# Kernel tuning notes

Hardware: AMD Instinct MI355X
Metric: run time of the kernel (lower is better)

The kernel has to match this reference:

```python
import jax, jax.numpy as jnp
import numpy as np

LN_EPS = 1e-12


def setup_inputs() -> dict:
    key = jax.random.key(0)
    ks = jax.random.split(key, 6)
    B, S, H = 32, 512, 768
    P, K = 76, 64
    V, E = 50257, 768
    return {
        "sequence_data": jax.random.normal(ks[0], (B, S, H), dtype=jnp.float32),
        "masked_positions": jax.random.randint(ks[1], (B, P), 0, S, dtype=jnp.int64),
        "candidate_sets": jax.random.randint(ks[2], (B, P, K), 0, V, dtype=jnp.int64),
        "embedding_table": jax.random.normal(ks[3], (V, E), dtype=jnp.float32) * 0.02,
        "dense_w": jax.random.normal(ks[4], (H, E), dtype=jnp.float32) * (1.0 / np.sqrt(H)),
        "dense_b": jnp.zeros((E,), dtype=jnp.float32),
        "ln_gamma": jnp.ones((E,), dtype=jnp.float32),
        "ln_beta": jnp.zeros((E,), dtype=jnp.float32),
    }


def reference(sequence_data, masked_positions, candidate_sets, embedding_table,
              dense_w, dense_b, ln_gamma, ln_beta):
    # Gather masked positions: [B, P, H]
    gathered = jnp.take_along_axis(
        sequence_data, masked_positions[:, :, None], axis=1)
    # Dense (no activation), then LayerNorm (eps=1e-12)
    lm = jnp.einsum('bph,he->bpe', gathered, dense_w) + dense_b
    mu = jnp.mean(lm, axis=-1, keepdims=True)
    var = jnp.mean(jnp.square(lm - mu), axis=-1, keepdims=True)
    lm = (lm - mu) * jax.lax.rsqrt(var + LN_EPS) * ln_gamma + ln_beta
    # Candidate embedding gather: [B, P, K, E]
    cand = embedding_table[candidate_sets]
    # Inner products -> logits [B, P, K]
    logits = jnp.einsum('bpe,bpke->bpk', lm, cand)
    return logits
```

## Files before the change

kernel.cpp:

```cpp
#include <hip/hip_runtime.h>

typedef __attribute__((ext_vector_type(8))) short bf16x8;
typedef __attribute__((ext_vector_type(4))) float f32x4;

#define HH 768
#define EE 768
#define BB 32
#define SS 512
#define PP 76
#define KCAND 64
#define MM (BB * PP)
#define VV 50257

#define OFF_WT    0u
#define OFF_AG    1179648u
#define OFF_LM    4915200u

#define WT_BLOCKS 576
#define AG_BLOCKS 304
#define GEMM_BLOCKS 456

__device__ inline unsigned short f2bf(float f) {
    unsigned int u = __float_as_uint(f);
    u += 0x7fffu + ((u >> 16) & 1u);
    return (unsigned short)(u >> 16);
}
__device__ inline float bf2f(unsigned short h) {
    return __uint_as_float(((unsigned int)h) << 16);
}

__global__ __launch_bounds__(256) void prep_kernel(
    const float* __restrict__ W, unsigned short* __restrict__ Wt,
    const float* __restrict__ seq, const int* __restrict__ mpos,
    unsigned short* __restrict__ Ag) {
    const int bid = blockIdx.x;
    if (bid < WT_BLOCKS) {
        __shared__ float tile[32][33];
        const int h0 = (bid % 24) * 32, e0 = (bid / 24) * 32;
        const int c = threadIdx.x & 31, r = threadIdx.x >> 5;
#pragma unroll
        for (int rr = r; rr < 32; rr += 8)
            tile[rr][c] = W[(size_t)(h0 + rr) * EE + e0 + c];
        __syncthreads();
#pragma unroll
        for (int rr = r; rr < 32; rr += 8)
            Wt[(size_t)(e0 + rr) * HH + h0 + c] = f2bf(tile[c][rr]);
    } else {
        const int m0 = (bid - WT_BLOCKS) * 8;
        const int t = threadIdx.x;
#pragma unroll
        for (int rr = 0; rr < 8; ++rr) {
            const int m = m0 + rr;
            const int b = m / PP, p = m - b * PP;
            const int ps = mpos[b * PP + p];
            const float* srow = seq + (size_t)(b * SS + ps) * HH;
            unsigned short* drow = Ag + (size_t)m * HH;
#pragma unroll
            for (int j = 0; j < 3; ++j)
                drow[t + j * 256] = f2bf(srow[t + j * 256]);
        }
    }
}

__global__ __launch_bounds__(256) void gemm_kernel(
    const unsigned short* __restrict__ Ag, const unsigned short* __restrict__ Wt,
    float* __restrict__ lm) {
    __shared__ unsigned short Alds[64][72];
    __shared__ unsigned short Blds[64][72];
    const int bid = blockIdx.x;
    const int bn = bid % 12, bm = bid / 12;
    const int tid = threadIdx.x;
    const int sr = tid >> 2, sc = (tid & 3) * 16;
    const unsigned short* abase = Ag + (size_t)(bm * 64) * HH;
    const unsigned short* bbase = Wt + (size_t)(bn * 64) * HH;
    const int lane = tid & 63, wv = tid >> 6;
    const int wm = wv >> 1, wn = wv & 1;
    const int fr = lane & 15, fq = (lane >> 4) * 8;
    f32x4 acc[2][2] = {};
    for (int kk = 0; kk < HH; kk += 64) {
        __syncthreads();
        *(int4*)&Alds[sr][sc]     = *(const int4*)(abase + (size_t)sr * HH + kk + sc);
        *(int4*)&Alds[sr][sc + 8] = *(const int4*)(abase + (size_t)sr * HH + kk + sc + 8);
        *(int4*)&Blds[sr][sc]     = *(const int4*)(bbase + (size_t)sr * HH + kk + sc);
        *(int4*)&Blds[sr][sc + 8] = *(const int4*)(bbase + (size_t)sr * HH + kk + sc + 8);
        __syncthreads();
#pragma unroll
        for (int ks = 0; ks < 64; ks += 32) {
            bf16x8 af[2], bfr[2];
#pragma unroll
            for (int t = 0; t < 2; ++t)
                af[t] = *(const bf16x8*)&Alds[wm * 32 + t * 16 + fr][ks + fq];
#pragma unroll
            for (int t = 0; t < 2; ++t)
                bfr[t] = *(const bf16x8*)&Blds[wn * 32 + t * 16 + fr][ks + fq];
#pragma unroll
            for (int tm = 0; tm < 2; ++tm)
#pragma unroll
                for (int tn = 0; tn < 2; ++tn)
                    acc[tm][tn] = __builtin_amdgcn_mfma_f32_16x16x32_bf16(
                        af[tm], bfr[tn], acc[tm][tn], 0, 0, 0);
        }
    }
#pragma unroll
    for (int tm = 0; tm < 2; ++tm)
#pragma unroll
        for (int tn = 0; tn < 2; ++tn) {
            const int col = bn * 64 + wn * 32 + tn * 16 + (lane & 15);
            const int rbase = bm * 64 + wm * 32 + tm * 16 + (lane >> 4) * 4;
#pragma unroll
            for (int g = 0; g < 4; ++g)
                lm[(size_t)(rbase + g) * EE + col] = acc[tm][tn][g];
        }
}

__global__ __launch_bounds__(256, 2) void mrow_logits_kernel(
    const float* __restrict__ lm, const float* __restrict__ bias,
    const float* __restrict__ gamma, const float* __restrict__ beta,
    const int* __restrict__ cand, const float* __restrict__ emb,
    float* __restrict__ out) {
    const int m = blockIdx.x;
    const int t = threadIdx.x;
    __shared__ unsigned short lmn_s[EE];
    __shared__ float redS[4], redQ[4];
    __shared__ int cand_s[KCAND];

    if (t < KCAND) cand_s[t] = cand[m * KCAND + t];

    const float x0 = lm[(size_t)m * EE + t]       + bias[t];
    const float x1 = lm[(size_t)m * EE + t + 256] + bias[t + 256];
    const float x2 = lm[(size_t)m * EE + t + 512] + bias[t + 512];
    float s = x0 + x1 + x2;
    float q = x0 * x0 + x1 * x1 + x2 * x2;
#pragma unroll
    for (int w = 32; w; w >>= 1) { s += __shfl_xor(s, w); q += __shfl_xor(q, w); }
    const int lane = t & 63, wv = t >> 6;
    if (lane == 0) { redS[wv] = s; redQ[wv] = q; }
    __syncthreads();
    s = redS[0] + redS[1] + redS[2] + redS[3];
    q = redQ[0] + redQ[1] + redQ[2] + redQ[3];
    const float mu = s * (1.0f / 768.0f);
    const float rstd = rsqrtf(q * (1.0f / 768.0f) - mu * mu + 1e-12f);
    lmn_s[t]       = f2bf((x0 - mu) * rstd * gamma[t]       + beta[t]);
    lmn_s[t + 256] = f2bf((x1 - mu) * rstd * gamma[t + 256] + beta[t + 256]);
    lmn_s[t + 512] = f2bf((x2 - mu) * rstd * gamma[t + 512] + beta[t + 512]);
    __syncthreads();

    const int g = t >> 4, l16 = t & 15;
    ushort4 ln4[12];
#pragma unroll
    for (int j = 0; j < 12; ++j)
        ln4[j] = *(const ushort4*)&lmn_s[4 * l16 + 64 * j];

    const f32x4* e4 = (const f32x4*)emb;
    const int cb = m * KCAND + g;
    const f32x4* p0 = e4 + (size_t)cand_s[g]      * 192 + l16;
    const f32x4* p1 = e4 + (size_t)cand_s[g + 16] * 192 + l16;
    const f32x4* p2 = e4 + (size_t)cand_s[g + 32] * 192 + l16;
    const f32x4* p3 = e4 + (size_t)cand_s[g + 48] * 192 + l16;
    f32x4 A0[12], A1[12], A2[12], A3[12];
#pragma unroll
    for (int j = 0; j < 12; ++j) A0[j] = p0[16 * j];
#pragma unroll
    for (int j = 0; j < 12; ++j) A1[j] = p1[16 * j];
#pragma unroll
    for (int j = 0; j < 12; ++j) A2[j] = p2[16 * j];
#pragma unroll
    for (int j = 0; j < 12; ++j) A3[j] = p3[16 * j];
    __builtin_amdgcn_sched_barrier(0);

    float d0 = 0.f, d1 = 0.f, d2 = 0.f, d3 = 0.f;
    float f0 = 0.f, f1 = 0.f, f2 = 0.f, f3 = 0.f;
#pragma unroll
    for (int j = 0; j < 12; j += 2) {
        float la[4], lb[4];
        la[0] = bf2f(ln4[j].x);     la[1] = bf2f(ln4[j].y);
        la[2] = bf2f(ln4[j].z);     la[3] = bf2f(ln4[j].w);
        lb[0] = bf2f(ln4[j + 1].x); lb[1] = bf2f(ln4[j + 1].y);
        lb[2] = bf2f(ln4[j + 1].z); lb[3] = bf2f(ln4[j + 1].w);
        d0 += la[0]*A0[j][0] + la[1]*A0[j][1] + la[2]*A0[j][2] + la[3]*A0[j][3];
        d1 += la[0]*A1[j][0] + la[1]*A1[j][1] + la[2]*A1[j][2] + la[3]*A1[j][3];
        d2 += la[0]*A2[j][0] + la[1]*A2[j][1] + la[2]*A2[j][2] + la[3]*A2[j][3];
        d3 += la[0]*A3[j][0] + la[1]*A3[j][1] + la[2]*A3[j][2] + la[3]*A3[j][3];
        f0 += lb[0]*A0[j+1][0] + lb[1]*A0[j+1][1] + lb[2]*A0[j+1][2] + lb[3]*A0[j+1][3];
        f1 += lb[0]*A1[j+1][0] + lb[1]*A1[j+1][1] + lb[2]*A1[j+1][2] + lb[3]*A1[j+1][3];
        f2 += lb[0]*A2[j+1][0] + lb[1]*A2[j+1][1] + lb[2]*A2[j+1][2] + lb[3]*A2[j+1][3];
        f3 += lb[0]*A3[j+1][0] + lb[1]*A3[j+1][1] + lb[2]*A3[j+1][2] + lb[3]*A3[j+1][3];
    }
    d0 += f0; d1 += f1; d2 += f2; d3 += f3;
#pragma unroll
    for (int w = 1; w < 16; w <<= 1) {
        d0 += __shfl_xor(d0, w); d1 += __shfl_xor(d1, w);
        d2 += __shfl_xor(d2, w); d3 += __shfl_xor(d3, w);
    }
    if (l16 == 0) {
        out[cb]      = d0;
        out[cb + 16] = d1;
        out[cb + 32] = d2;
        out[cb + 48] = d3;
    }
}

extern "C" void kernel_launch(void* const* d_in, const int* in_sizes, int n_in,
                              void* d_out, int out_size, void* d_ws, size_t ws_size,
                              hipStream_t stream) {
    const float* seq   = (const float*)d_in[0];
    const int*   mpos  = (const int*)d_in[1];
    const int*   cand  = (const int*)d_in[2];
    const float* emb   = (const float*)d_in[3];
    const float* W     = (const float*)d_in[4];
    const float* bias  = (const float*)d_in[5];
    const float* gamma = (const float*)d_in[6];
    const float* beta  = (const float*)d_in[7];
    float* out = (float*)d_out;

    char* ws = (char*)d_ws;
    unsigned short* Wt = (unsigned short*)(ws + OFF_WT);
    unsigned short* Ag = (unsigned short*)(ws + OFF_AG);
    float*          lm = (float*)(ws + OFF_LM);

    prep_kernel<<<WT_BLOCKS + AG_BLOCKS, 256, 0, stream>>>(W, Wt, seq, mpos, Ag);
    gemm_kernel<<<GEMM_BLOCKS, 256, 0, stream>>>(Ag, Wt, lm);
    mrow_logits_kernel<<<MM, 256, 0, stream>>>(lm, bias, gamma, beta, cand, emb, out);
}
```

Before: 292.0 us.

## Convert embedding table to bf16 alongside GEMM and gather bf16 rows

Adds conversion blocks to the GEMM launch that cast the full fp32 embedding table to bf16 in workspace. The logits kernel then gathers candidate rows as bf16 vectors, halving bytes per gathered row. This trades a full-table streaming read and write each call for cheaper random gathers, and it adds bf16 rounding on the embeddings. The logits kernel also drops its occupancy hint.

```diff
diff --git a/kernel.cpp b/kernel.cpp
--- a/kernel.cpp
+++ b/kernel.cpp
@@ -15,10 +15,12 @@
 #define OFF_WT    0u
 #define OFF_AG    1179648u
 #define OFF_LM    4915200u
+#define OFF_EMB   12386304u
 
 #define WT_BLOCKS 576
 #define AG_BLOCKS 304
 #define GEMM_BLOCKS 456
+#define CONV_BLOCKS 18847
 
 __device__ inline unsigned short f2bf(float f) {
     unsigned int u = __float_as_uint(f);
@@ -62,12 +64,25 @@
     }
 }
 
-__global__ __launch_bounds__(256) void gemm_kernel(
+__global__ __launch_bounds__(256) void gemm_conv_kernel(
     const unsigned short* __restrict__ Ag, const unsigned short* __restrict__ Wt,
-    float* __restrict__ lm) {
-    __shared__ unsigned short Alds[64][72];
-    __shared__ unsigned short Blds[64][72];
+    float* __restrict__ lm, const float* __restrict__ embf,
+    unsigned short* __restrict__ embB) {
     const int bid = blockIdx.x;
+    if (bid >= GEMM_BLOCKS) {
+        const size_t i = ((size_t)(bid - GEMM_BLOCKS) * 2048) + (size_t)threadIdx.x * 8;
+        if (i < (size_t)VV * EE) {
+            const float4 a = *(const float4*)(embf + i);
+            const float4 b = *(const float4*)(embf + i + 4);
+            unsigned short o[8];
+            o[0] = f2bf(a.x); o[1] = f2bf(a.y); o[2] = f2bf(a.z); o[3] = f2bf(a.w);
+            o[4] = f2bf(b.x); o[5] = f2bf(b.y); o[6] = f2bf(b.z); o[7] = f2bf(b.w);
+            *(int4*)(embB + i) = *(const int4*)o;
+        }
+        return;
+    }
+    __shared__ __align__(16) unsigned short Alds[64][72];
+    __shared__ __align__(16) unsigned short Blds[64][72];
     const int bn = bid % 12, bm = bid / 12;
     const int tid = threadIdx.x;
     const int sr = tid >> 2, sc = (tid & 3) * 16;
@@ -113,14 +128,14 @@
         }
 }
 
-__global__ __launch_bounds__(256, 2) void mrow_logits_kernel(
+__global__ __launch_bounds__(256) void mrow_logits_kernel(
     const float* __restrict__ lm, const float* __restrict__ bias,
     const float* __restrict__ gamma, const float* __restrict__ beta,
-    const int* __restrict__ cand, const float* __restrict__ emb,
+    const int* __restrict__ cand, const unsigned short* __restrict__ embB,
     float* __restrict__ out) {
     const int m = blockIdx.x;
     const int t = threadIdx.x;
-    __shared__ unsigned short lmn_s[EE];
+    __shared__ __align__(16) unsigned short lmn_s[EE];
     __shared__ float redS[4], redQ[4];
     __shared__ int cand_s[KCAND];
 
@@ -146,45 +161,49 @@
     __syncthreads();
 
     const int g = t >> 4, l16 = t & 15;
-    ushort4 ln4[12];
-#pragma unroll
-    for (int j = 0; j < 12; ++j)
-        ln4[j] = *(const ushort4*)&lmn_s[4 * l16 + 64 * j];
-
-    const f32x4* e4 = (const f32x4*)emb;
+    bf16x8 ln8[6];
+#pragma unroll
+    for (int j = 0; j < 6; ++j)
+        ln8[j] = *(const bf16x8*)&lmn_s[8 * l16 + 128 * j];
+
+    const bf16x8* e8 = (const bf16x8*)embB;
     const int cb = m * KCAND + g;
-    const f32x4* p0 = e4 + (size_t)cand_s[g]      * 192 + l16;
-    const f32x4* p1 = e4 + (size_t)cand_s[g + 16] * 192 + l16;
-    const f32x4* p2 = e4 + (size_t)cand_s[g + 32] * 192 + l16;
-    const f32x4* p3 = e4 + (size_t)cand_s[g + 48] * 192 + l16;
-    f32x4 A0[12], A1[12], A2[12], A3[12];
-#pragma unroll
-    for (int j = 0; j < 12; ++j) A0[j] = p0[16 * j];
-#pragma unroll
-    for (int j = 0; j < 12; ++j) A1[j] = p1[16 * j];
-#pragma unroll
-    for (int j = 0; j < 12; ++j) A2[j] = p2[16 * j];
-#pragma unroll
-    for (int j = 0; j < 12; ++j) A3[j] = p3[16 * j];
+    const bf16x8* p0 = e8 + (size_t)cand_s[g]      * 96 + l16;
+    const bf16x8* p1 = e8 + (size_t)cand_s[g + 16] * 96 + l16;
+    const bf16x8* p2 = e8 + (size_t)cand_s[g + 32] * 96 + l16;
+    const bf16x8* p3 = e8 + (size_t)cand_s[g + 48] * 96 + l16;
+    bf16x8 A0[6], A1[6], A2[6], A3[6];
+#pragma unroll
+    for (int j = 0; j < 6; ++j) A0[j] = p0[16 * j];
+#pragma unroll
+    for (int j = 0; j < 6; ++j) A1[j] = p1[16 * j];
+#pragma unroll
+    for (int j = 0; j < 6; ++j) A2[j] = p2[16 * j];
+#pragma unroll
+    for (int j = 0; j < 6; ++j) A3[j] = p3[16 * j];
     __builtin_amdgcn_sched_barrier(0);
 
     float d0 = 0.f, d1 = 0.f, d2 = 0.f, d3 = 0.f;
     float f0 = 0.f, f1 = 0.f, f2 = 0.f, f3 = 0.f;
 #pragma unroll
-    for (int j = 0; j < 12; j += 2) {
-        float la[4], lb[4];
-        la[0] = bf2f(ln4[j].x);     la[1] = bf2f(ln4[j].y);
-        la[2] = bf2f(ln4[j].z);     la[3] = bf2f(ln4[j].w);
-        lb[0] = bf2f(ln4[j + 1].x); lb[1] = bf2f(ln4[j + 1].y);
-        lb[2] = bf2f(ln4[j + 1].z); lb[3] = bf2f(ln4[j + 1].w);
-        d0 += la[0]*A0[j][0] + la[1]*A0[j][1] + la[2]*A0[j][2] + la[3]*A0[j][3];
-        d1 += la[0]*A1[j][0] + la[1]*A1[j][1] + la[2]*A1[j][2] + la[3]*A1[j][3];
-        d2 += la[0]*A2[j][0] + la[1]*A2[j][1] + la[2]*A2[j][2] + la[3]*A2[j][3];
-        d3 += la[0]*A3[j][0] + la[1]*A3[j][1] + la[2]*A3[j][2] + la[3]*A3[j][3];
-        f0 += lb[0]*A0[j+1][0] + lb[1]*A0[j+1][1] + lb[2]*A0[j+1][2] + lb[3]*A0[j+1][3];
-        f1 += lb[0]*A1[j+1][0] + lb[1]*A1[j+1][1] + lb[2]*A1[j+1][2] + lb[3]*A1[j+1][3];
-        f2 += lb[0]*A2[j+1][0] + lb[1]*A2[j+1][1] + lb[2]*A2[j+1][2] + lb[3]*A2[j+1][3];
-        f3 += lb[0]*A3[j+1][0] + lb[1]*A3[j+1][1] + lb[2]*A3[j+1][2] + lb[3]*A3[j+1][3];
+    for (int j = 0; j < 6; ++j) {
+        float lv[8];
+#pragma unroll
+        for (int e = 0; e < 8; ++e) lv[e] = bf2f((unsigned short)ln8[j][e]);
+#pragma unroll
+        for (int e = 0; e < 4; ++e) {
+            d0 += lv[e] * bf2f((unsigned short)A0[j][e]);
+            d1 += lv[e] * bf2f((unsigned short)A1[j][e]);
+            d2 += lv[e] * bf2f((unsigned short)A2[j][e]);
+            d3 += lv[e] * bf2f((unsigned short)A3[j][e]);
+        }
+#pragma unroll
+        for (int e = 4; e < 8; ++e) {
+            f0 += lv[e] * bf2f((unsigned short)A0[j][e]);
+            f1 += lv[e] * bf2f((unsigned short)A1[j][e]);
+            f2 += lv[e] * bf2f((unsigned short)A2[j][e]);
+            f3 += lv[e] * bf2f((unsigned short)A3[j][e]);
+        }
     }
     d0 += f0; d1 += f1; d2 += f2; d3 += f3;
 #pragma unroll
@@ -214,11 +233,13 @@
     float* out = (float*)d_out;
 
     char* ws = (char*)d_ws;
-    unsigned short* Wt = (unsigned short*)(ws + OFF_WT);
-    unsigned short* Ag = (unsigned short*)(ws + OFF_AG);
-    float*          lm = (float*)(ws + OFF_LM);
+    unsigned short* Wt   = (unsigned short*)(ws + OFF_WT);
+    unsigned short* Ag   = (unsigned short*)(ws + OFF_AG);
+    float*          lm   = (float*)(ws + OFF_LM);
+    unsigned short* embB = (unsigned short*)(ws + OFF_EMB);
 
     prep_kernel<<<WT_BLOCKS + AG_BLOCKS, 256, 0, stream>>>(W, Wt, seq, mpos, Ag);
-    gemm_kernel<<<GEMM_BLOCKS, 256, 0, stream>>>(Ag, Wt, lm);
-    mrow_logits_kernel<<<MM, 256, 0, stream>>>(lm, bias, gamma, beta, cand, emb, out);
-}
+    gemm_conv_kernel<<<GEMM_BLOCKS + CONV_BLOCKS, 256, 0, stream>>>(
+        Ag, Wt, lm, emb, embB);
+    mrow_logits_kernel<<<MM, 256, 0, stream>>>(lm, bias, gamma, beta, cand, embB, out);
+}
```

Measured after the change: 297.4 us. Within noise of the previous version (+1.8%).
